# Performance work log

Measured on AMD Instinct MI355X. Metric: run time of the kernel, lower is better.

The kernel has to match this reference:

```python
import jax, jax.numpy as jnp
import numpy as np

N, D = 1024, 128
C = 1.0                 # curvature c
MIN_NORM = 1e-15
PROJ_EPS = 4e-3         # HGCN float32 projection eps


def _artanh(x):
    return jnp.arctanh(jnp.clip(x, -1.0 + 1e-7, 1.0 - 1e-7))


def _lambda_x(x, c):
    x2 = jnp.sum(x * x, axis=-1, keepdims=True)
    return 2.0 / jnp.clip(1.0 - c * x2, MIN_NORM)


def _mobius_add(x, y, c):
    x2 = jnp.sum(x * x, axis=-1, keepdims=True)
    y2 = jnp.sum(y * y, axis=-1, keepdims=True)
    xy = jnp.sum(x * y, axis=-1, keepdims=True)
    num = (1.0 + 2.0 * c * xy + c * y2) * x + (1.0 - c * x2) * y
    den = 1.0 + 2.0 * c * xy + c * c * x2 * y2
    return num / jnp.clip(den, MIN_NORM)


def _logmap0(p, c):
    sqrt_c = c ** 0.5
    pn = jnp.clip(jnp.linalg.norm(p, axis=-1, keepdims=True), MIN_NORM)
    return (_artanh(sqrt_c * pn) / (sqrt_c * pn)) * p


def _logmap(p1, p2, c):
    # log map of p2 in the tangent space at p1 (broadcasts)
    sub = _mobius_add(-p1, p2, c)
    sn = jnp.clip(jnp.linalg.norm(sub, axis=-1, keepdims=True), MIN_NORM)
    lam = _lambda_x(p1, c)
    sqrt_c = c ** 0.5
    return (2.0 / (sqrt_c * lam)) * _artanh(sqrt_c * sn) * sub / sn


def _expmap(p, u, c):
    # exp map of tangent vector u at point p
    sqrt_c = c ** 0.5
    un = jnp.clip(jnp.linalg.norm(u, axis=-1, keepdims=True), MIN_NORM)
    second = jnp.tanh(0.5 * sqrt_c * _lambda_x(p, c) * un) * u / (sqrt_c * un)
    return _mobius_add(p, second, c)


def _proj(x, c):
    n = jnp.clip(jnp.linalg.norm(x, axis=-1, keepdims=True), MIN_NORM)
    maxnorm = (1.0 - PROJ_EPS) / (c ** 0.5)
    return jnp.where(n > maxnorm, x / n * maxnorm, x)


def setup_inputs() -> dict:
    key = jax.random.key(0)
    k1, k2, k3, k4 = jax.random.split(key, 4)
    # points inside the Poincare ball (norm ~ 0.05*sqrt(D) ~ 0.57 < 1)
    x = 0.05 * jax.random.normal(k1, (N, D), dtype=jnp.float32)
    adj = jax.random.uniform(k2, (N, N), dtype=jnp.float32)
    # DenseAtt: Linear(2*D -> 1)
    att_w = jax.random.normal(k3, (2 * D,), dtype=jnp.float32) / np.sqrt(2.0 * D)
    att_b = 0.01 * jax.random.normal(k4, (), dtype=jnp.float32)
    return {"x": x, "adj": adj, "att_w": att_w, "att_b": att_b}


def reference(x, adj, att_w, att_b):
    c = C
    d = x.shape[-1]
    x_tan = _logmap0(x, c)                               # [N, d]
    # per-node local tangents: logmap_{x_i}(x_j) for all i, j -> [N, N, d]
    x_loc = _logmap(x[:, None, :], x[None, :, :], c)
    # DenseAtt: sigmoid(Linear(cat(x_i, x_j))) * adj, decomposed to avoid [N,N,2d]
    left = x_tan @ att_w[:d]                             # [N]
    right = x_tan @ att_w[d:]                            # [N]
    att = jax.nn.sigmoid(left[:, None] + right[None, :] + att_b) * adj  # [N, N]
    support_t = jnp.einsum('ij,ijd->id', att, x_loc)     # [N, d]
    return _proj(_expmap(x, support_t, c), c)
```

## Files before the change

kernel.cpp:

```cpp
#include <hip/hip_runtime.h>

#define NN 1024
#define DD 128

__device__ __forceinline__ float frcp(float x) {
  return __builtin_amdgcn_rcpf(x);
}
__device__ __forceinline__ float fsqrt(float x) {
  return __builtin_amdgcn_sqrtf(x);
}
__device__ __forceinline__ float artanh_ratio(float z) {
  z = fminf(z, 1.0f - 1e-7f);
  if (z < 1e-4f) return 1.0f + z * z * (1.0f / 3.0f);
  return 0.5f * (__logf(1.0f + z) - __logf(1.0f - z)) * frcp(z);
}
__device__ __forceinline__ float ftanh(float a) {
  const float e = __expf(-2.0f * a);
  return (1.0f - e) * frcp(1.0f + e);
}

__global__ __launch_bounds__(512) void k23_pairs_v(
    const float* __restrict__ x, const float* __restrict__ adj,
    const float* __restrict__ aw, const float* __restrict__ bptr,
    float* __restrict__ Vp, float* __restrict__ PA) {
  __shared__ __align__(16) float xiT[DD * 64];
  __shared__ __align__(16) float xjT[DD * 64];
  __shared__ float s_nx2i[64], s_lft[64], s_nx2j[64], s_rgt[64];
  const int t = threadIdx.x;
  const int bi = blockIdx.y, bj = blockIdx.x;
  const int tx = t & 15;
  const int ty = t >> 4;
  const int gi0 = bi * 64 + ty * 2;
  const int gj0 = bj * 64 + tx * 4;

  float4 ajv[2];
#pragma unroll
  for (int i = 0; i < 2; ++i)
    ajv[i] = *(const float4*)&adj[(size_t)(gi0 + i) * NN + gj0];
  const float attb = bptr[0];

  {
    const int r = t & 63;
    const int kq = t >> 6;
    const float* si = x + (bi * 64 + r) * DD + kq * 16;
    const float* sj = x + (bj * 64 + r) * DD + kq * 16;
#pragma unroll
    for (int m = 0; m < 4; ++m) {
      const int k0 = kq * 16 + m * 4;
      const float4 vi = *(const float4*)(si + m * 4);
      const float4 vj = *(const float4*)(sj + m * 4);
      xiT[(k0 + 0) * 64 + r] = vi.x;
      xiT[(k0 + 1) * 64 + r] = vi.y;
      xiT[(k0 + 2) * 64 + r] = vi.z;
      xiT[(k0 + 3) * 64 + r] = vi.w;
      xjT[(k0 + 0) * 64 + r] = vj.x;
      xjT[(k0 + 1) * 64 + r] = vj.y;
      xjT[(k0 + 2) * 64 + r] = vj.z;
      xjT[(k0 + 3) * 64 + r] = vj.w;
    }
  }
  __syncthreads();

  {
    const int r = (t >> 2) & 63;
    const int h = t & 3;
    const bool jp = (t >= 256);
    const float* panel = jp ? xjT : xiT;
    const float* wv = aw + (jp ? DD : 0);
    float sa = 0.0f, sb = 0.0f;
    const int k0 = h * 32;
#pragma unroll 8
    for (int k = 0; k < 32; ++k) {
      const float v = panel[(k0 + k) * 64 + r];
      sa = fmaf(v, v, sa);
      sb = fmaf(v, wv[k0 + k], sb);
    }
    sa += __shfl_xor(sa, 1, 64);
    sb += __shfl_xor(sb, 1, 64);
    sa += __shfl_xor(sa, 2, 64);
    sb += __shfl_xor(sb, 2, 64);
    if (h == 0) {
      const float pn = fmaxf(fsqrt(sa), 1e-15f);
      const float hh = artanh_ratio(pn);
      if (jp) { s_nx2j[r] = sa; s_rgt[r] = hh * sb; }
      else    { s_nx2i[r] = sa; s_lft[r] = hh * sb; }
    }
  }
  __syncthreads();

  float acc[2][4] = {};
#pragma unroll 2
  for (int kb = 0; kb < DD; kb += 4) {
    float2 A[4];
    float4 B[4];
#pragma unroll
    for (int q = 0; q < 4; ++q) {
      A[q] = *(const float2*)&xiT[(kb + q) * 64 + ty * 2];
      B[q] = *(const float4*)&xjT[(kb + q) * 64 + tx * 4];
    }
#pragma unroll
    for (int q = 0; q < 4; ++q) {
      acc[0][0] = fmaf(A[q].x, B[q].x, acc[0][0]);
      acc[0][1] = fmaf(A[q].x, B[q].y, acc[0][1]);
      acc[0][2] = fmaf(A[q].x, B[q].z, acc[0][2]);
      acc[0][3] = fmaf(A[q].x, B[q].w, acc[0][3]);
      acc[1][0] = fmaf(A[q].y, B[q].x, acc[1][0]);
      acc[1][1] = fmaf(A[q].y, B[q].y, acc[1][1]);
      acc[1][2] = fmaf(A[q].y, B[q].z, acc[1][2]);
      acc[1][3] = fmaf(A[q].y, B[q].w, acc[1][3]);
    }
  }

  float ny2v[4], rv[4];
#pragma unroll
  for (int j = 0; j < 4; ++j) {
    ny2v[j] = s_nx2j[tx * 4 + j];
    rv[j] = s_rgt[tx * 4 + j];
  }
  float4 ureg[2];
  float sua[2];
#pragma unroll
  for (int i = 0; i < 2; ++i) {
    const float xi2 = s_nx2i[ty * 2 + i];
    const float li = s_lft[ty * 2 + i];
    const float beta = 1.0f - xi2;
    const float betac = fmaxf(beta, 1e-15f);
    const float av[4] = {ajv[i].x, ajv[i].y, ajv[i].z, ajv[i].w};
    float u4[4];
    float ua = 0.0f;
#pragma unroll
    for (int j = 0; j < 4; ++j) {
      const float s = acc[i][j];
      const float al = 1.0f - 2.0f * s + ny2v[j];
      const float den = fmaxf(1.0f - 2.0f * s + xi2 * ny2v[j], 1e-15f);
      const float rden = frcp(den);
      float s2 = fmaxf(al * al * xi2 - 2.0f * al * beta * s + beta * beta * ny2v[j], 0.0f);
      s2 = s2 * rden * rden;
      const float sn = fmaxf(fsqrt(s2), 1e-15f);
      const float G = betac * artanh_ratio(sn);
      const float sig = frcp(1.0f + __expf(-(li + rv[j] + attb)));
      const float u = sig * av[j] * G * rden;
      u4[j] = u;
      ua = fmaf(u, al, ua);
    }
    ureg[i].x = u4[0]; ureg[i].y = u4[1]; ureg[i].z = u4[2]; ureg[i].w = u4[3];
    sua[i] = ua;
  }
#pragma unroll
  for (int m = 1; m < 16; m <<= 1) {
#pragma unroll
    for (int i = 0; i < 2; ++i) sua[i] += __shfl_xor(sua[i], m, 64);
  }
  if (tx == 0) {
#pragma unroll
    for (int i = 0; i < 2; ++i) PA[(gi0 + i) * 16 + bj] = sua[i];
  }

  __syncthreads();
  float* u_lds = xiT;
#pragma unroll
  for (int i = 0; i < 2; ++i)
    *(float4*)&u_lds[(ty * 2 + i) * 64 + tx * 4] = ureg[i];
  __syncthreads();

  {
    const int tx2 = t & 31, ty2 = t >> 5;
    const int i0 = ty2 * 4, d0 = tx2 * 4;
    float4 a4[4];
#pragma unroll
    for (int ii = 0; ii < 4; ++ii) a4[ii] = make_float4(0.0f, 0.0f, 0.0f, 0.0f);
#pragma unroll 4
    for (int jb = 0; jb < 16; ++jb) {
      const int j0 = jb * 4;
      float4 xv[4];
#pragma unroll
      for (int jj = 0; jj < 4; ++jj)
        xv[jj] = *(const float4*)&x[(size_t)(bj * 64 + j0 + jj) * DD + d0];
      float4 uv[4];
#pragma unroll
      for (int ii = 0; ii < 4; ++ii)
        uv[ii] = *(const float4*)&u_lds[(i0 + ii) * 64 + j0];
#pragma unroll
      for (int ii = 0; ii < 4; ++ii) {
        a4[ii].x = fmaf(uv[ii].x, xv[0].x, fmaf(uv[ii].y, xv[1].x, fmaf(uv[ii].z, xv[2].x, fmaf(uv[ii].w, xv[3].x, a4[ii].x))));
        a4[ii].y = fmaf(uv[ii].x, xv[0].y, fmaf(uv[ii].y, xv[1].y, fmaf(uv[ii].z, xv[2].y, fmaf(uv[ii].w, xv[3].y, a4[ii].y))));
        a4[ii].z = fmaf(uv[ii].x, xv[0].z, fmaf(uv[ii].y, xv[1].z, fmaf(uv[ii].z, xv[2].z, fmaf(uv[ii].w, xv[3].z, a4[ii].z))));
        a4[ii].w = fmaf(uv[ii].x, xv[0].w, fmaf(uv[ii].y, xv[1].w, fmaf(uv[ii].z, xv[2].w, fmaf(uv[ii].w, xv[3].w, a4[ii].w))));
      }
    }
#pragma unroll
    for (int ii = 0; ii < 4; ++ii)
      *(float4*)&Vp[((size_t)bj * NN + bi * 64 + i0 + ii) * DD + d0] = a4[ii];
  }
}

__global__ __launch_bounds__(256) void k4_final(
    const float* __restrict__ x, const float* __restrict__ Vp,
    const float* __restrict__ PA, float* __restrict__ out) {
  const int t = threadIdx.x;
  const int w = t >> 6;
  const int l = t & 63;
  const int row = blockIdx.x * 4 + w;

  const float2 xv = *(const float2*)&x[row * DD + 2 * l];
  const float xi0 = xv.x, xi1 = xv.y;
  float ra = xi0 * xi0 + xi1 * xi1;
#pragma unroll
  for (int m = 1; m < 64; m <<= 1) ra += __shfl_xor(ra, m, 64);
  const float nx2i = ra;

  float v0 = 0.0f, v1 = 0.0f;
#pragma unroll
  for (int kt = 0; kt < 16; ++kt) {
    const float2 vv = *(const float2*)&Vp[((size_t)kt * NN + row) * DD + 2 * l];
    v0 += vv.x;
    v1 += vv.y;
  }
  float sa = (l < 16) ? PA[row * 16 + l] : 0.0f;
#pragma unroll
  for (int m = 1; m < 64; m <<= 1) sa += __shfl_xor(sa, m, 64);

  const float beta = 1.0f - nx2i;
  const float betac = fmaxf(beta, 1e-15f);
  const float u0 = beta * v0 - sa * xi0;
  const float u1 = beta * v1 - sa * xi1;
  float p0 = u0 * u0 + u1 * u1;
  float p1 = xi0 * u0 + xi1 * u1;
#pragma unroll
  for (int m = 1; m < 64; m <<= 1) {
    p0 += __shfl_xor(p0, m, 64);
    p1 += __shfl_xor(p1, m, 64);
  }
  const float un = fmaxf(fsqrt(p0), 1e-15f);
  const float tau = ftanh(frcp(betac) * un) * frcp(un);
  const float y2 = tau * tau * p0;
  const float xy = tau * p1;
  const float numx = 1.0f + 2.0f * xy + y2;
  const float dene = fmaxf(1.0f + 2.0f * xy + nx2i * y2, 1e-15f);
  const float rdene = frcp(dene);
  float r0 = (numx * xi0 + beta * tau * u0) * rdene;
  float r1 = (numx * xi1 + beta * tau * u1) * rdene;
  const float n2 = fmaxf(numx * numx * nx2i + 2.0f * numx * beta * xy + beta * beta * y2, 0.0f);
  const float n = fmaxf(fsqrt(n2) * rdene, 1e-15f);
  const float maxn = 1.0f - 4e-3f;
  if (n > maxn) {
    const float sc = maxn * frcp(n);
    r0 *= sc;
    r1 *= sc;
  }
  float2 ro; ro.x = r0; ro.y = r1;
  *(float2*)&out[row * DD + 2 * l] = ro;
}

__global__ __launch_bounds__(256) void hypagg_fused(
    const float* __restrict__ x, const float* __restrict__ adj,
    const float* __restrict__ aw, const float* __restrict__ bptr,
    float* __restrict__ out) {
  __shared__ __align__(16) float xi_lds[4 * DD];
  __shared__ __align__(16) float w2_lds[DD];
  const int t = threadIdx.x;
  const int w = t >> 6;
  const int l = t & 63;
  const int row = blockIdx.x * 4 + w;

  xi_lds[t] = x[blockIdx.x * 4 * DD + t];
  xi_lds[t + 256] = x[blockIdx.x * 4 * DD + t + 256];
  if (t < DD) w2_lds[t] = aw[DD + t];
  __syncthreads();

  const float attb = bptr[0];
  const float* xi = &xi_lds[w * DD];
  const float xi0 = xi[l];
  const float xi1 = xi[l + 64];

  float ra = xi0 * xi0 + xi1 * xi1;
  float rb = xi0 * aw[l] + xi1 * aw[l + 64];
#pragma unroll
  for (int m = 1; m < 64; m <<= 1) {
    ra += __shfl_xor(ra, m, 64);
    rb += __shfl_xor(rb, m, 64);
  }
  const float nx2i = ra;
  const float beta = 1.0f - nx2i;
  const float betac = fmaxf(beta, 1e-15f);
  const float hi = artanh_ratio(fmaxf(fsqrt(nx2i), 1e-15f));
  const float lfti = hi * rb;

  float V0 = 0.0f, V1 = 0.0f, SA = 0.0f;

  for (int j0 = 0; j0 < NN; j0 += 64) {
    const int jj = j0 + l;
    const float* xj = x + jj * DD;
    float s = 0.0f, ny2 = 0.0f, rj = 0.0f;
#pragma unroll 8
    for (int k4 = 0; k4 < DD / 4; ++k4) {
      const float4 b4 = *(const float4*)(xj + k4 * 4);
      const float4 a4 = *(const float4*)(xi + k4 * 4);
      const float4 w4 = *(const float4*)(&w2_lds[k4 * 4]);
      s   = fmaf(a4.x, b4.x, fmaf(a4.y, b4.y, fmaf(a4.z, b4.z, fmaf(a4.w, b4.w, s))));
      ny2 = fmaf(b4.x, b4.x, fmaf(b4.y, b4.y, fmaf(b4.z, b4.z, fmaf(b4.w, b4.w, ny2))));
      rj  = fmaf(w4.x, b4.x, fmaf(w4.y, b4.y, fmaf(w4.z, b4.z, fmaf(w4.w, b4.w, rj))));
    }
    const float hj = artanh_ratio(fmaxf(fsqrt(ny2), 1e-15f));
    const float rgtj = hj * rj;
    const float al = 1.0f - 2.0f * s + ny2;
    const float den = fmaxf(1.0f - 2.0f * s + nx2i * ny2, 1e-15f);
    const float rden = frcp(den);
    float s2 = fmaxf(al * al * nx2i - 2.0f * al * beta * s + beta * beta * ny2, 0.0f);
    s2 = s2 * rden * rden;
    const float sn = fmaxf(fsqrt(s2), 1e-15f);
    const float G = betac * artanh_ratio(sn);
    const float sig = frcp(1.0f + __expf(-(lfti + rgtj + attb)));
    const float u = sig * adj[row * NN + jj] * G * rden;
    SA = fmaf(u, al, SA);
#pragma unroll 16
    for (int jq = 0; jq < 64; ++jq) {
      const float uq = __shfl(u, jq, 64);
      const float xd0 = x[(j0 + jq) * DD + l];
      const float xd1 = x[(j0 + jq) * DD + l + 64];
      V0 = fmaf(uq, xd0, V0);
      V1 = fmaf(uq, xd1, V1);
    }
  }

#pragma unroll
  for (int m = 1; m < 64; m <<= 1) SA += __shfl_xor(SA, m, 64);

  const float u0 = beta * V0 - SA * xi0;
  const float u1 = beta * V1 - SA * xi1;
  float p0 = u0 * u0 + u1 * u1;
  float p1 = xi0 * u0 + xi1 * u1;
#pragma unroll
  for (int m = 1; m < 64; m <<= 1) {
    p0 += __shfl_xor(p0, m, 64);
    p1 += __shfl_xor(p1, m, 64);
  }
  const float un = fmaxf(fsqrt(p0), 1e-15f);
  const float tau = ftanh(frcp(betac) * un) * frcp(un);
  const float y2 = tau * tau * p0;
  const float xy = tau * p1;
  const float numx = 1.0f + 2.0f * xy + y2;
  const float dene = fmaxf(1.0f + 2.0f * xy + nx2i * y2, 1e-15f);
  const float rdene = frcp(dene);
  float r0 = (numx * xi0 + beta * tau * u0) * rdene;
  float r1 = (numx * xi1 + beta * tau * u1) * rdene;
  const float n2 = fmaxf(numx * numx * nx2i + 2.0f * numx * beta * xy + beta * beta * y2, 0.0f);
  const float n = fmaxf(fsqrt(n2) * rdene, 1e-15f);
  const float maxn = 1.0f - 4e-3f;
  if (n > maxn) {
    const float sc = maxn * frcp(n);
    r0 *= sc;
    r1 *= sc;
  }
  out[row * DD + l] = r0;
  out[row * DD + l + 64] = r1;
}

extern "C" void kernel_launch(void* const* d_in, const int* in_sizes, int n_in,
                              void* d_out, int out_size, void* d_ws, size_t ws_size,
                              hipStream_t stream) {
  const float* x = nullptr;
  const float* adj = nullptr;
  const float* aw = nullptr;
  const float* ab = nullptr;
  for (int i = 0; i < n_in; ++i) {
    switch (in_sizes[i]) {
      case NN * DD:  x   = (const float*)d_in[i]; break;
      case NN * NN:  adj = (const float*)d_in[i]; break;
      case 2 * DD:   aw  = (const float*)d_in[i]; break;
      case 1:        ab  = (const float*)d_in[i]; break;
      default: break;
    }
  }
  float* out = (float*)d_out;

  const size_t need = (16 * (size_t)NN * DD + NN * 16) * sizeof(float);
  if (ws_size >= need) {
    float* Vp = (float*)d_ws;
    float* PA = Vp + 16 * (size_t)NN * DD;
    hipLaunchKernelGGL(k23_pairs_v, dim3(16, 16), dim3(512), 0, stream,
                       x, adj, aw, ab, Vp, PA);
    hipLaunchKernelGGL(k4_final, dim3(NN / 4), dim3(256), 0, stream,
                       x, Vp, PA, out);
  } else {
    hipLaunchKernelGGL(hypagg_fused, dim3(NN / 4), dim3(256), 0, stream,
                       x, adj, aw, ab, out);
  }
}
```

Measured before the change: 28.14 us.

## Fuse final expmap/proj stage into pair kernel via per-row-block atomic counters

```diff
diff --git a/kernel.cpp b/kernel.cpp
--- a/kernel.cpp
+++ b/kernel.cpp
@@ -19,10 +19,11 @@
   return (1.0f - e) * frcp(1.0f + e);
 }
 
-__global__ __launch_bounds__(512) void k23_pairs_v(
+__global__ __launch_bounds__(512) void mega2(
     const float* __restrict__ x, const float* __restrict__ adj,
     const float* __restrict__ aw, const float* __restrict__ bptr,
-    float* __restrict__ Vp, float* __restrict__ PA) {
+    float* __restrict__ Vp, float* __restrict__ PA,
+    unsigned* __restrict__ cnt, float* __restrict__ out) {
   __shared__ __align__(16) float xiT[DD * 64];
   __shared__ __align__(16) float xjT[DD * 64];
   __shared__ float s_nx2i[64], s_lft[64], s_nx2j[64], s_rgt[64];
@@ -192,64 +193,77 @@
     for (int ii = 0; ii < 4; ++ii)
       *(float4*)&Vp[((size_t)bj * NN + bi * 64 + i0 + ii) * DD + d0] = a4[ii];
   }
-}
-
-__global__ __launch_bounds__(256) void k4_final(
-    const float* __restrict__ x, const float* __restrict__ Vp,
-    const float* __restrict__ PA, float* __restrict__ out) {
-  const int t = threadIdx.x;
-  const int w = t >> 6;
-  const int l = t & 63;
-  const int row = blockIdx.x * 4 + w;
-
-  const float2 xv = *(const float2*)&x[row * DD + 2 * l];
-  const float xi0 = xv.x, xi1 = xv.y;
-  float ra = xi0 * xi0 + xi1 * xi1;
-#pragma unroll
-  for (int m = 1; m < 64; m <<= 1) ra += __shfl_xor(ra, m, 64);
-  const float nx2i = ra;
-
-  float v0 = 0.0f, v1 = 0.0f;
-#pragma unroll
-  for (int kt = 0; kt < 16; ++kt) {
-    const float2 vv = *(const float2*)&Vp[((size_t)kt * NN + row) * DD + 2 * l];
-    v0 += vv.x;
-    v1 += vv.y;
-  }
-  float sa = (l < 16) ? PA[row * 16 + l] : 0.0f;
-#pragma unroll
-  for (int m = 1; m < 64; m <<= 1) sa += __shfl_xor(sa, m, 64);
-
-  const float beta = 1.0f - nx2i;
-  const float betac = fmaxf(beta, 1e-15f);
-  const float u0 = beta * v0 - sa * xi0;
-  const float u1 = beta * v1 - sa * xi1;
-  float p0 = u0 * u0 + u1 * u1;
-  float p1 = xi0 * u0 + xi1 * u1;
-#pragma unroll
-  for (int m = 1; m < 64; m <<= 1) {
-    p0 += __shfl_xor(p0, m, 64);
-    p1 += __shfl_xor(p1, m, 64);
-  }
-  const float un = fmaxf(fsqrt(p0), 1e-15f);
-  const float tau = ftanh(frcp(betac) * un) * frcp(un);
-  const float y2 = tau * tau * p0;
-  const float xy = tau * p1;
-  const float numx = 1.0f + 2.0f * xy + y2;
-  const float dene = fmaxf(1.0f + 2.0f * xy + nx2i * y2, 1e-15f);
-  const float rdene = frcp(dene);
-  float r0 = (numx * xi0 + beta * tau * u0) * rdene;
-  float r1 = (numx * xi1 + beta * tau * u1) * rdene;
-  const float n2 = fmaxf(numx * numx * nx2i + 2.0f * numx * beta * xy + beta * beta * y2, 0.0f);
-  const float n = fmaxf(fsqrt(n2) * rdene, 1e-15f);
-  const float maxn = 1.0f - 4e-3f;
-  if (n > maxn) {
-    const float sc = maxn * frcp(n);
-    r0 *= sc;
-    r1 *= sc;
-  }
-  float2 ro; ro.x = r0; ro.y = r1;
-  *(float2*)&out[row * DD + 2 * l] = ro;
+
+  __syncthreads();
+  if (t == 0) {
+    __threadfence();
+    atomicAdd(&cnt[bi], 1u);
+  }
+  if (bj >= 4) return;
+
+  if (t == 0) {
+    while (__hip_atomic_load(&cnt[bi], __ATOMIC_RELAXED, __HIP_MEMORY_SCOPE_AGENT) < 16u)
+      __builtin_amdgcn_s_sleep(2);
+    __threadfence();
+  }
+  __syncthreads();
+
+  {
+    const int l = t & 63;
+    const int w8 = t >> 6;
+#pragma unroll
+    for (int r = 0; r < 2; ++r) {
+      const int row = bi * 64 + bj * 16 + w8 * 2 + r;
+      const float2 xv = *(const float2*)&x[row * DD + 2 * l];
+      const float xi0 = xv.x, xi1 = xv.y;
+      float ra = xi0 * xi0 + xi1 * xi1;
+#pragma unroll
+      for (int m = 1; m < 64; m <<= 1) ra += __shfl_xor(ra, m, 64);
+      const float nx2i = ra;
+
+      float v0 = 0.0f, v1 = 0.0f;
+#pragma unroll
+      for (int kt = 0; kt < 16; ++kt) {
+        const float2 vv = *(const float2*)&Vp[((size_t)kt * NN + row) * DD + 2 * l];
+        v0 += vv.x;
+        v1 += vv.y;
+      }
+      float sa = (l < 16) ? PA[row * 16 + l] : 0.0f;
+#pragma unroll
+      for (int m = 1; m < 64; m <<= 1) sa += __shfl_xor(sa, m, 64);
+
+      const float beta = 1.0f - nx2i;
+      const float betac = fmaxf(beta, 1e-15f);
+      const float u0 = beta * v0 - sa * xi0;
+      const float u1 = beta * v1 - sa * xi1;
+      float p0 = u0 * u0 + u1 * u1;
+      float p1 = xi0 * u0 + xi1 * u1;
+#pragma unroll
+      for (int m = 1; m < 64; m <<= 1) {
+        p0 += __shfl_xor(p0, m, 64);
+        p1 += __shfl_xor(p1, m, 64);
+      }
+      const float un = fmaxf(fsqrt(p0), 1e-15f);
+      const float tau = ftanh(frcp(betac) * un) * frcp(un);
+      const float y2 = tau * tau * p0;
+      const float xy = tau * p1;
+      const float numx = 1.0f + 2.0f * xy + y2;
+      const float dene = fmaxf(1.0f + 2.0f * xy + nx2i * y2, 1e-15f);
+      const float rdene = frcp(dene);
+      float r0 = (numx * xi0 + beta * tau * u0) * rdene;
+      float r1 = (numx * xi1 + beta * tau * u1) * rdene;
+      const float n2 = fmaxf(numx * numx * nx2i + 2.0f * numx * beta * xy + beta * beta * y2, 0.0f);
+      const float n = fmaxf(fsqrt(n2) * rdene, 1e-15f);
+      const float maxn = 1.0f - 4e-3f;
+      if (n > maxn) {
+        const float sc = maxn * frcp(n);
+        r0 *= sc;
+        r1 *= sc;
+      }
+      float2 ro; ro.x = r0; ro.y = r1;
+      *(float2*)&out[row * DD + 2 * l] = ro;
+    }
+  }
 }
 
 __global__ __launch_bounds__(256) void hypagg_fused(
@@ -374,14 +388,14 @@
   }
   float* out = (float*)d_out;
 
-  const size_t need = (16 * (size_t)NN * DD + NN * 16) * sizeof(float);
+  const size_t need = (16 * (size_t)NN * DD + NN * 16) * sizeof(float) + 16 * sizeof(unsigned);
   if (ws_size >= need) {
     float* Vp = (float*)d_ws;
     float* PA = Vp + 16 * (size_t)NN * DD;
-    hipLaunchKernelGGL(k23_pairs_v, dim3(16, 16), dim3(512), 0, stream,
-                       x, adj, aw, ab, Vp, PA);
-    hipLaunchKernelGGL(k4_final, dim3(NN / 4), dim3(256), 0, stream,
-                       x, Vp, PA, out);
+    unsigned* cnt = (unsigned*)(PA + NN * 16);
+    hipMemsetAsync((void*)cnt, 0, 16 * sizeof(unsigned), stream);
+    hipLaunchKernelGGL(mega2, dim3(16, 16), dim3(512), 0, stream,
+                       x, adj, aw, ab, Vp, PA, cnt, out);
   } else {
     hipLaunchKernelGGL(hypagg_fused, dim3(NN / 4), dim3(256), 0, stream,
                        x, adj, aw, ab, out);
```

After: 48.37 us. 1.72x slower.
